# Performance work log

Hardware: AMD Instinct MI355X
Metric: run time of the kernel (lower is better)

## Reference

```python
import jax, jax.numpy as jnp
import numpy as np

KS = 3          # kernel_size
C_IN = 64       # channel_size
F_OUT = 128     # filters
K_CONNECT = 4   # n_connect (<= KS*KS)
N_POS = KS * KS


def setup_inputs() -> dict:
    key = jax.random.key(0)
    k1, k2, k3, k4 = jax.random.split(key, 4)
    x = jax.random.normal(k1, (16, 128, 128, C_IN), dtype=jnp.float32)
    kern = jax.random.normal(k2, (KS, KS, C_IN, F_OUT), dtype=jnp.float32) * 0.1  # he_uniform-ish
    b = jnp.zeros((F_OUT,), dtype=jnp.float32)
    D = jax.random.normal(k3, (KS, KS, C_IN, F_OUT), dtype=jnp.float32) * 0.5     # trainable logits
    gumbel_u = jax.random.uniform(k4, (1, F_OUT, C_IN, N_POS), dtype=jnp.float32)  # BS=1 uniform noise
    return {"x": x, "kern": kern, "b": b, "D": D, "gumbel_u": gumbel_u}


def dps_topk(D, u, k, temp):
    # D: [KS, KS, C, F]; raw reshape to [F, C, KS*KS] exactly as the TF code does
    F_, C_ = D.shape[3], D.shape[2]
    N_ = D.shape[0] * D.shape[0]
    logits = D.reshape(F_, C_, N_)                       # [F, C, N]
    gn = -0.001 * jnp.log(-jnp.log(u + 1e-20) + 1e-20)   # [1, F, C, N] scaled Gumbel noise
    pert = logits[None] + gn                             # [1, F, C, N]
    # top-k by value (descending), then top-k of the indices -> indices sorted descending
    _, idx = jax.lax.top_k(pert, k)                      # [1, F, C, k] int32
    idx_desc, _ = jax.lax.top_k(idx, k)                  # sorted descending
    topk = idx_desc[..., ::-1]                           # ascending indices
    hard = jax.nn.one_hot(topk, N_, dtype=logits.dtype)  # [1, F, C, k, N]
    cum = jnp.cumsum(hard, axis=-2) - hard               # exclusive cumsum over k (hard is 0/1)
    prob_exp = jnp.exp(logits)[None, :, :, None, :]      # [1, F, C, 1, N] broadcast over k
    soft = jax.nn.softmax(
        (jnp.log(prob_exp * (1.0 - cum + 1e-20)) + gn[:, :, :, None, :]) / temp,
        axis=-1,
    )
    # straight-through: hard forward, soft backward
    return jax.lax.stop_gradient(hard - soft) + soft


def reference(x, kern, b, D, gumbel_u):
    temp = 1.0  # step=0 -> epoch=0 -> initial temperature
    A_ = dps_topk(D, gumbel_u, K_CONNECT, temp)          # [1, F, C, k, N]
    A = A_[0].sum(axis=-2).reshape(KS, KS, C_IN, F_OUT)  # raw reshape, as in the TF code
    # binarize kernel with straight-through estimator
    t1 = jnp.sign(kern)
    t2 = jnp.clip(0.4 * kern, -1.0, 1.0)                 # 2*hard_sigmoid(k) - 1
    ww = jax.lax.stop_gradient(t1 - t2) + t2
    AW = A * ww                                          # sparse-masked binary kernel
    y = jax.lax.conv_general_dilated(
        x, AW, window_strides=(1, 1), padding='SAME',
        dimension_numbers=('NHWC', 'HWIO', 'NHWC'),
    )
    y = y + b
    return jax.nn.relu(y)
```

## Files before the change

### kernel.cpp

```cpp
#include <hip/hip_runtime.h>
#include <hip/hip_bf16.h>
#include <math.h>

#define KS 3
#define C_IN 64
#define F_OUT 128
#define NPOS 9
#define HH 128
#define WWID 128
#define NB 16

typedef __attribute__((ext_vector_type(8))) short bf16x8;
typedef __attribute__((ext_vector_type(4))) float f32x4;

__device__ __forceinline__ unsigned short f2bf(float f) {
  union { float f; unsigned u; } v; v.f = f;
  unsigned u = v.u;
  return (unsigned short)((u + 0x7FFFu + ((u >> 16) & 1u)) >> 16);
}
__device__ __forceinline__ unsigned cvtpk(float lo, float hi) {
  unsigned r;
  asm("v_cvt_pk_bf16_f32 %0, %1, %2" : "=v"(r) : "v"(lo), "v"(hi));
  return r;
}
__device__ __forceinline__ bf16x8 pack8(float4 v0, float4 v1) {
  union { unsigned u[4]; bf16x8 v; } r;
  r.u[0] = cvtpk(v0.x, v0.y); r.u[1] = cvtpk(v0.z, v0.w);
  r.u[2] = cvtpk(v1.x, v1.y); r.u[3] = cvtpk(v1.z, v1.w);
  return r.v;
}
__device__ __forceinline__ void gload16(const void* g, void* l) {
  __builtin_amdgcn_global_load_lds(
      (const __attribute__((address_space(1))) unsigned int*)g,
      (__attribute__((address_space(3))) unsigned int*)l, 16, 0, 0);
}

__global__ void compute_aw(const float* __restrict__ kern,
                           const float* __restrict__ D,
                           const float* __restrict__ gu,
                           unsigned short* __restrict__ AWsw) {
  int t = blockIdx.x * blockDim.x + threadIdx.x;
  if (t >= F_OUT * C_IN) return;
  int base = t * NPOS;
  float pert[NPOS];
#pragma unroll
  for (int n = 0; n < NPOS; ++n) {
    float u = gu[base + n];
    float g = -0.001f * logf(-logf(u + 1e-20f) + 1e-20f);
    pert[n] = D[base + n] + g;
  }
  unsigned mask = 0;
#pragma unroll
  for (int k = 0; k < 4; ++k) {
    int best = 0; float bv = -INFINITY;
#pragma unroll
    for (int n = 0; n < NPOS; ++n) {
      bool taken = (mask >> n) & 1;
      if (!taken && pert[n] > bv) { bv = pert[n]; best = n; }
    }
    mask |= (1u << best);
  }
#pragma unroll
  for (int n = 0; n < NPOS; ++n) {
    int L = base + n;
    float kv = kern[L];
    float sg = (kv > 0.f) ? 1.f : ((kv < 0.f) ? -1.f : 0.f);
    float v = ((mask >> n) & 1) ? sg : 0.f;
    int f = L & (F_OUT - 1);
    int r = L >> 7;
    int c = r & (C_IN - 1);
    int p = r >> 6;
    int s = p / 3, pl = p % 3;
    int g = c >> 3;
    int slot = g ^ (f & 7);
    int off = s * 24576 + ((pl * F_OUT + f) * 8 + slot) * 8 + (c & 7);
    AWsw[off] = f2bf(v);
  }
}

__global__ __launch_bounds__(1024, 4)
void conv6(const float* __restrict__ x,
           const unsigned short* __restrict__ AWsw,
           const float* __restrict__ bias,
           float* __restrict__ out) {
  __shared__ __align__(16) unsigned short As[6 * 130 * 64];
  __shared__ __align__(16) unsigned short Bs[3 * F_OUT * 64];

  int tid = threadIdx.x;
  int lane = tid & 63, wave = tid >> 6;
  int lr = lane & 15, lg = lane >> 4;

  int bid = blockIdx.x;
  int wg = (bid & 7) * 64 + (bid >> 3);
  int n = wg >> 5;
  int h0 = (wg & 31) * 4;

  int ro = wave >> 2;
  int m0 = ((wave >> 1) & 1) * 64;
  int f0 = (wave & 1) * 64;

  bf16x8 z = {};
  if (h0 == 0 || h0 == 124) {
    for (int t = tid; t < 6240; t += 1024)
      *reinterpret_cast<bf16x8*>(As + t * 8) = z;
  } else if (tid < 96) {
    int r = tid >> 4, k = tid & 15;
    int pp = (k >> 3) ? 129 : 0, c8 = k & 7;
    *reinterpret_cast<bf16x8*>((char*)As + r * 16640 + pp * 128 +
                               ((c8 ^ (pp & 7)) << 4)) = z;
  }
  __syncthreads();

#pragma unroll
  for (int k = 0; k < 3; ++k) {
    int wi = wave * 3 + k;
    gload16(AWsw + wi * 512 + lane * 8, (char*)Bs + wi * 1024);
  }

  const float* xim = x + ((long long)n * HH) * WWID * C_IN;
#pragma unroll
  for (int t = 0; t < 6; ++t) {
    int cid = t * 1024 + tid;
    int r = cid >> 10, rem = cid & 1023;
    int px = rem >> 3, c8 = rem & 7;
    int hh = h0 - 1 + r;
    if ((unsigned)hh < (unsigned)HH) {
      const float* sp = xim + (long long)hh * (WWID * C_IN) + px * C_IN + c8 * 8;
      float4 v0 = *reinterpret_cast<const float4*>(sp);
      float4 v1 = *reinterpret_cast<const float4*>(sp + 4);
      int pp = px + 1;
      *reinterpret_cast<bf16x8*>((char*)As + r * 16640 + pp * 128 +
                                 ((c8 ^ (pp & 7)) << 4)) = pack8(v0, v1);
    }
  }
  __syncthreads();

  f32x4 acc[4][4] = {};
  bf16x8 pre[3];

#define PREFETCH(SN)                                                         \
  _Pragma("unroll")                                                          \
  for (int k = 0; k < 3; ++k)                                                \
    pre[k] = *reinterpret_cast<const bf16x8*>(                               \
        AWsw + (SN) * 24576 + (k * 1024 + tid) * 8);

#define BWRITE()                                                             \
  _Pragma("unroll")                                                          \
  for (int k = 0; k < 3; ++k)                                                \
    *reinterpret_cast<bf16x8*>(Bs + (k * 1024 + tid) * 8) = pre[k];

#define COMPUTE(S)                                                           \
  __builtin_amdgcn_s_setprio(1);                                             \
  _Pragma("unroll")                                                          \
  for (int pl = 0; pl < 3; ++pl) {                                           \
    _Pragma("unroll")                                                        \
    for (int ch = 0; ch < 2; ++ch) {                                         \
      const char* bp = (const char*)Bs + pl * 16384 + (f0 << 7) + lr * 128 + \
                       (((ch * 4 + lg) ^ (lr & 7)) << 4);                    \
      bf16x8 b[4];                                                           \
      _Pragma("unroll")                                                      \
      for (int nf = 0; nf < 4; ++nf)                                         \
        b[nf] = *reinterpret_cast<const bf16x8*>(bp + nf * 2048);            \
      bf16x8 a[4];                                                           \
      _Pragma("unroll")                                                      \
      for (int mfi = 0; mfi < 4; ++mfi) {                                    \
        int pxb = m0 + mfi * 16 + lr + pl;                                   \
        a[mfi] = *reinterpret_cast<const bf16x8*>(                           \
            (const char*)As + (ro + (S)) * 16640 + pxb * 128 +               \
            (((ch * 4 + lg) ^ (pxb & 7)) << 4));                             \
      }                                                                      \
      _Pragma("unroll")                                                      \
      for (int mfi = 0; mfi < 4; ++mfi)                                      \
        _Pragma("unroll")                                                    \
        for (int nf = 0; nf < 4; ++nf)                                       \
          acc[mfi][nf] = __builtin_amdgcn_mfma_f32_16x16x32_bf16(            \
              a[mfi], b[nf], acc[mfi][nf], 0, 0, 0);                         \
    }                                                                        \
  }                                                                          \
  __builtin_amdgcn_s_setprio(0);

  PREFETCH(1)
  COMPUTE(0)
  __syncthreads();
  BWRITE()
  __syncthreads();
  PREFETCH(2)
  COMPUTE(1)
  __syncthreads();
  BWRITE()
  __syncthreads();
  COMPUTE(2)

  float bi[4];
#pragma unroll
  for (int nf = 0; nf < 4; ++nf) bi[nf] = bias[f0 + nf * 16 + lr];
  int ho = h0 + ro;
  long long ob = ((long long)(n * HH + ho)) * WWID * F_OUT + f0 + lr;
#pragma unroll
  for (int mfi = 0; mfi < 4; ++mfi) {
#pragma unroll
    for (int r4 = 0; r4 < 4; ++r4) {
      int w = m0 + mfi * 16 + lg * 4 + r4;
      float* op = out + ob + (long long)w * F_OUT;
#pragma unroll
      for (int nf = 0; nf < 4; ++nf)
        op[nf * 16] = fmaxf(acc[mfi][nf][r4] + bi[nf], 0.f);
    }
  }
#undef PREFETCH
#undef BWRITE
#undef COMPUTE
}

extern "C" void kernel_launch(void* const* d_in, const int* in_sizes, int n_in,
                              void* d_out, int out_size, void* d_ws, size_t ws_size,
                              hipStream_t stream) {
  const float* x    = (const float*)d_in[0];
  const float* kern = (const float*)d_in[1];
  const float* bias = (const float*)d_in[2];
  const float* D    = (const float*)d_in[3];
  const float* gu   = (const float*)d_in[4];

  unsigned short* AWsw = (unsigned short*)d_ws;

  compute_aw<<<(F_OUT * C_IN + 255) / 256, 256, 0, stream>>>(kern, D, gu, AWsw);

  conv6<<<NB * (HH / 4), 1024, 0, stream>>>(x, AWsw, bias, (float*)d_out);
}
```

Baseline: 57.33 us.

## Overlap loading of last two input halo rows with MFMA compute stages

The conv kernel now loads only the first four input rows into LDS before compute starts. Rows 4 and 5 are fetched into registers while the first and second kernel-row stages run, then packed and written to LDS at the existing barriers. The first weight-slice load also moves ahead of the zero-fill, and one barrier is removed. This hides part of the global-load latency behind matrix math, at the cost of extra live registers and a clamped row index for the bottom boundary.

After: 76.48 us. 1.33x slower.

```diff
diff --git a/kernel.cpp b/kernel.cpp
--- a/kernel.cpp
+++ b/kernel.cpp
@@ -72,17 +72,16 @@
     int p = r >> 6;
     int s = p / 3, pl = p % 3;
     int g = c >> 3;
-    int slot = g ^ (f & 7);
-    int off = s * 24576 + ((pl * F_OUT + f) * 8 + slot) * 8 + (c & 7);
+    int off = s * 24576 + ((pl * F_OUT + f) * 8 + (g ^ (f & 7))) * 8 + (c & 7);
     AWsw[off] = f2bf(v);
   }
 }
 
 __global__ __launch_bounds__(1024, 4)
-void conv6(const float* __restrict__ x,
-           const unsigned short* __restrict__ AWsw,
-           const float* __restrict__ bias,
-           float* __restrict__ out) {
+void conv6b(const float* __restrict__ x,
+            const unsigned short* __restrict__ AWsw,
+            const float* __restrict__ bias,
+            float* __restrict__ out) {
   __shared__ __align__(16) unsigned short As[6 * 130 * 64];
   __shared__ __align__(16) unsigned short Bs[3 * F_OUT * 64];
 
@@ -98,6 +97,14 @@
   int ro = wave >> 2;
   int m0 = ((wave >> 1) & 1) * 64;
   int f0 = (wave & 1) * 64;
+
+  const float* xim = x + ((long long)n * HH) * WWID * C_IN;
+
+#pragma unroll
+  for (int k = 0; k < 3; ++k) {
+    int wi = wave * 3 + k;
+    gload16(AWsw + wi * 512 + lane * 8, (char*)Bs + wi * 1024);
+  }
 
   bf16x8 z = {};
   if (h0 == 0 || h0 == 124) {
@@ -109,17 +116,9 @@
     *reinterpret_cast<bf16x8*>((char*)As + r * 16640 + pp * 128 +
                                ((c8 ^ (pp & 7)) << 4)) = z;
   }
-  __syncthreads();
-
-#pragma unroll
-  for (int k = 0; k < 3; ++k) {
-    int wi = wave * 3 + k;
-    gload16(AWsw + wi * 512 + lane * 8, (char*)Bs + wi * 1024);
-  }
-
-  const float* xim = x + ((long long)n * HH) * WWID * C_IN;
-#pragma unroll
-  for (int t = 0; t < 6; ++t) {
+
+#pragma unroll
+  for (int t = 0; t < 4; ++t) {
     int cid = t * 1024 + tid;
     int r = cid >> 10, rem = cid & 1023;
     int px = rem >> 3, c8 = rem & 7;
@@ -137,6 +136,8 @@
 
   f32x4 acc[4][4] = {};
   bf16x8 pre[3];
+  float4 xr0, xr1;
+  int pxi = tid >> 3, c8i = tid & 7;
 
 #define PREFETCH(SN)                                                         \
   _Pragma("unroll")                                                          \
@@ -148,6 +149,25 @@
   _Pragma("unroll")                                                          \
   for (int k = 0; k < 3; ++k)                                                \
     *reinterpret_cast<bf16x8*>(Bs + (k * 1024 + tid) * 8) = pre[k];
+
+#define ISSUE_ROW(R)                                                         \
+  {                                                                          \
+    int hh = h0 - 1 + (R);                                                   \
+    int hc = hh > 127 ? 127 : hh;                                            \
+    const float* sp = xim + (long long)hc * (WWID * C_IN) + pxi * C_IN +     \
+                      c8i * 8;                                               \
+    xr0 = *reinterpret_cast<const float4*>(sp);                              \
+    xr1 = *reinterpret_cast<const float4*>(sp + 4);                          \
+  }
+
+#define DRAIN_ROW(R)                                                         \
+  {                                                                          \
+    int hh = h0 - 1 + (R);                                                   \
+    bf16x8 val = (hh < HH) ? pack8(xr0, xr1) : z;                            \
+    int pp = pxi + 1;                                                        \
+    *reinterpret_cast<bf16x8*>((char*)As + (R) * 16640 + pp * 128 +          \
+                               ((c8i ^ (pp & 7)) << 4)) = val;               \
+  }
 
 #define COMPUTE(S)                                                           \
   __builtin_amdgcn_s_setprio(1);                                             \
@@ -180,14 +200,18 @@
   __builtin_amdgcn_s_setprio(0);
 
   PREFETCH(1)
+  ISSUE_ROW(4)
   COMPUTE(0)
   __syncthreads();
   BWRITE()
+  DRAIN_ROW(4)
   __syncthreads();
   PREFETCH(2)
+  ISSUE_ROW(5)
   COMPUTE(1)
   __syncthreads();
   BWRITE()
+  DRAIN_ROW(5)
   __syncthreads();
   COMPUTE(2)
 
@@ -209,6 +233,8 @@
   }
 #undef PREFETCH
 #undef BWRITE
+#undef ISSUE_ROW
+#undef DRAIN_ROW
 #undef COMPUTE
 }
 
@@ -225,5 +251,5 @@
 
   compute_aw<<<(F_OUT * C_IN + 255) / 256, 256, 0, stream>>>(kern, D, gu, AWsw);
 
-  conv6<<<NB * (HH / 4), 1024, 0, stream>>>(x, AWsw, bias, (float*)d_out);
-}
+  conv6b<<<NB * (HH / 4), 1024, 0, stream>>>(x, AWsw, bias, (float*)d_out);
+}
```
